# Optimization experiments

Hardware: AMD Instinct MI355X
Metric: run time of the kernel (lower is better)

The kernel has to match this reference:

```python
import jax, jax.numpy as jnp
import numpy as np

N_CONV = 3
FEAT = 128
N_RBF = 20
CUTOFF = 5.0
EPS = 1e-15
N_NODES = 10000
N_EDGES = 160000


def setup_inputs() -> dict:
    key = jax.random.key(0)
    ks = jax.random.split(key, 8)
    N, E = N_NODES, N_EDGES
    cg_xyz = jax.random.normal(ks[0], (N, 3), jnp.float32) * 2.0
    # Directed, self-loop-free edge list (both i<j and i>j present, so the
    # original make_directed() is a no-op on this data).
    src = jax.random.randint(ks[1], (E,), 0, N)
    off = jax.random.randint(ks[2], (E,), 1, N)
    CG_nbr_list = jnp.stack([src, (src + off) % N], axis=1)
    cg_s = jax.random.normal(ks[3], (N, FEAT), jnp.float32)
    s = 1.0 / np.sqrt(FEAT)
    # Per-conv-layer weights of ENMessageBlock: inv_dense = Dense(F->F, silu) + Dense(F->3F);
    # dist_embed = ExpNormalBasis(n_rbf) -> Dense(n_rbf->3F) * cosine envelope.
    W1 = jax.random.normal(ks[4], (N_CONV, FEAT, FEAT), jnp.float32) * s
    b1 = jnp.zeros((N_CONV, FEAT), jnp.float32)
    W2 = jax.random.normal(ks[5], (N_CONV, FEAT, 3 * FEAT), jnp.float32) * s
    b2 = jnp.zeros((N_CONV, 3 * FEAT), jnp.float32)
    Wr = jax.random.normal(ks[6], (N_CONV, N_RBF, 3 * FEAT), jnp.float32) / np.sqrt(N_RBF)
    br = jnp.zeros((N_CONV, 3 * FEAT), jnp.float32)
    return {"cg_xyz": cg_xyz, "CG_nbr_list": CG_nbr_list, "cg_s": cg_s,
            "W1": W1, "b1": b1, "W2": W2, "b2": b2, "Wr": Wr, "br": br}


def _expnorm_rbf(dist):
    # ExpNormalBasis: exp(-beta * (exp(-d) - mu)^2), mu in [exp(-cutoff), 1]
    mu = jnp.linspace(np.exp(-CUTOFF), 1.0, N_RBF, dtype=jnp.float32)
    beta = np.float32((2.0 / N_RBF * (1.0 - np.exp(-CUTOFF))) ** -2)
    return jnp.exp(-beta * (jnp.exp(-dist)[:, None] - mu) ** 2)  # (E, n_rbf)


def _cos_envelope(dist):
    return jnp.where(dist < CUTOFF, 0.5 * (jnp.cos(jnp.pi * dist / CUTOFF) + 1.0), 0.0)


def reference(cg_xyz, CG_nbr_list, cg_s, W1, b1, W2, b2, Wr, br):
    N = cg_s.shape[0]
    i, j = CG_nbr_list[:, 0], CG_nbr_list[:, 1]
    r_ij = cg_xyz[j] - cg_xyz[i]                      # (E, 3)
    dist = jnp.sqrt((r_ij ** 2 + EPS).sum(-1))        # (E,)
    unit = r_ij / dist[:, None]                        # (E, 3)
    rbf = _expnorm_rbf(dist)                           # (E, n_rbf) edge-invariant across layers
    env = _cos_envelope(dist)[:, None]                 # (E, 1)

    s_i = cg_s                                         # (N, F)
    v_i = jnp.zeros((N, FEAT, 3), cg_s.dtype)          # (N, F, 3)
    for l in range(N_CONV):
        phi = jax.nn.silu(s_i @ W1[l] + b1[l]) @ W2[l] + b2[l]   # (N, 3F)
        w_s = (rbf @ Wr[l] + br[l]) * env                         # (E, 3F)
        prod = phi[j] * w_s                                       # (E, 3F) gather + gate
        ds = prod[:, :FEAT]                                       # scalar message
        gate_v = prod[:, FEAT:2 * FEAT]                           # gates v_j
        gate_u = prod[:, 2 * FEAT:]                               # gates unit vector
        dv_ij = gate_u[:, :, None] * unit[:, None, :] + gate_v[:, :, None] * v_i[j]  # (E, F, 3)
        s_i = s_i + jax.ops.segment_sum(ds, i, num_segments=N)
        v_i = v_i + jax.ops.segment_sum(dv_ij, i, num_segments=N)
    return s_i, v_i
```

## Files before the change

### kernel.cpp

```cpp
#include <hip/hip_runtime.h>
#include <hip/hip_bf16.h>

#define NRBF 20
#define KAUG 32

typedef __attribute__((ext_vector_type(8))) short short8;
typedef __attribute__((ext_vector_type(4))) float float4v;
typedef __attribute__((ext_vector_type(2))) _Float16 half2v;
typedef __attribute__((ext_vector_type(8))) _Float16 half8v;
typedef unsigned short ushort_t;

union H8 { half8v v8; half2v v2[4]; };

__device__ __forceinline__ float bf2f(ushort_t u) {
    return __uint_as_float(((unsigned)u) << 16);
}
__device__ __forceinline__ ushort_t f2bf(float f) {
    unsigned u = __float_as_uint(f);
    u += 0x7FFF + ((u >> 16) & 1);
    return (ushort_t)(u >> 16);
}
__device__ __forceinline__ float ldin(const void* p, size_t idx, int isbf) {
    return isbf ? bf2f(((const ushort_t*)p)[idx]) : ((const float*)p)[idx];
}
__device__ __forceinline__ void stout(void* p, size_t idx, float v, int isbf) {
    if (isbf) ((ushort_t*)p)[idx] = f2bf(v);
    else      ((float*)p)[idx] = v;
}
__device__ __forceinline__ float dot2(half2v a, half2v b, float c) {
#if __has_builtin(__builtin_amdgcn_fdot2)
    return __builtin_amdgcn_fdot2(a, b, c, false);
#else
    return c + (float)a.x * (float)b.x + (float)a.y * (float)b.y;
#endif
}

__global__ void detect_kernel(const void* __restrict__ xyz, int* __restrict__ flag,
                              int* __restrict__ deg, int N) {
    int idx = blockIdx.x * blockDim.x + threadIdx.x;
    if (idx < N) deg[idx] = 0;
    if (blockIdx.x == 0 && threadIdx.x < 64) {
        const ushort_t* u = (const ushort_t*)xyz;
        unsigned e0 = (u[2 * threadIdx.x] >> 7) & 0xFF;
        unsigned long long bad = __ballot(e0 >= 0x90);
        if (threadIdx.x == 0) *flag = (__popcll(bad) > 2) ? 0 : 1;
    }
}

__global__ void prelude_kernel(const void* __restrict__ xyz, const int* __restrict__ nbr,
                               const void* __restrict__ cg_s,
                               const void* __restrict__ W1, const void* __restrict__ W2,
                               const void* __restrict__ Wr, const void* __restrict__ br,
                               float* __restrict__ s_acc, ushort_t* __restrict__ s_hi,
                               ushort_t* __restrict__ s_lo, int* __restrict__ deg,
                               ushort_t* __restrict__ B1hi, ushort_t* __restrict__ B1lo,
                               ushort_t* __restrict__ B2hi, ushort_t* __restrict__ B2lo,
                               _Float16* __restrict__ WrT,
                               int N128, int E, const int* __restrict__ flagp) {
    int isbf = *flagp;
    int idx = blockIdx.x * blockDim.x + threadIdx.x;
    if (idx < E) {
        int i = nbr[2 * idx], j = nbr[2 * idx + 1];
        float dx = ldin(xyz, 3 * j,     isbf) - ldin(xyz, 3 * i,     isbf);
        float dy = ldin(xyz, 3 * j + 1, isbf) - ldin(xyz, 3 * i + 1, isbf);
        float dz = ldin(xyz, 3 * j + 2, isbf) - ldin(xyz, 3 * i + 2, isbf);
        float dist = sqrtf(dx * dx + dy * dy + dz * dz + 3e-15f);
        if (dist < 5.0f) atomicAdd(&deg[i], 1);
    }
    if (idx < N128) {
        float v = ldin(cg_s, idx, isbf);
        s_acc[idx] = v;
        ushort_t hi = f2bf(v);
        s_hi[idx] = hi;
        s_lo[idx] = f2bf(v - bf2f(hi));
    }
    const int NW1 = 3 * 4 * 8 * 64;
    const int NW2 = 3 * 4 * 24 * 64;
    const int NWT = 3 * 384;
    if (idx < NW1) {
        int lane = idx & 63;
        int t = idx >> 6;
        int nt = t % 8; t /= 8;
        int ks = t % 4; int l = t / 4;
        int n = lane & 15, quad = lane >> 4;
        int col = nt * 16 + n;
        size_t base = (size_t)l * 128 * 128;
        size_t fo = (size_t)idx * 8;
        #pragma unroll
        for (int j = 0; j < 8; j++) {
            int k = ks * 32 + quad * 8 + j;
            float v = ldin(W1, base + (size_t)k * 128 + col, isbf);
            ushort_t hi = f2bf(v);
            B1hi[fo + j] = hi;
            B1lo[fo + j] = f2bf(v - bf2f(hi));
        }
    } else if (idx < NW1 + NW2) {
        int i2 = idx - NW1;
        int lane = i2 & 63;
        int t = i2 >> 6;
        int nt = t % 24; t /= 24;
        int ks = t % 4; int l = t / 4;
        int n = lane & 15, quad = lane >> 4;
        int col = nt * 16 + n;
        size_t base = (size_t)l * 128 * 384;
        size_t fo = (size_t)i2 * 8;
        #pragma unroll
        for (int j = 0; j < 8; j++) {
            int k = ks * 32 + quad * 8 + j;
            float v = ldin(W2, base + (size_t)k * 384 + col, isbf);
            ushort_t hi = f2bf(v);
            B2hi[fo + j] = hi;
            B2lo[fo + j] = f2bf(v - bf2f(hi));
        }
    } else if (idx < NW1 + NW2 + NWT) {
        int i2 = idx - NW1 - NW2;
        int l = i2 / 384, col = i2 % 384;
        _Float16* wt = WrT + ((size_t)l * 384 + col) * KAUG;
        #pragma unroll
        for (int k = 0; k < KAUG; k++) {
            float v = 0.f;
            if (k < NRBF) v = ldin(Wr, ((size_t)l * NRBF + k) * 384 + col, isbf);
            else if (k == NRBF) v = ldin(br, (size_t)l * 384 + col, isbf);
            wt[k] = (_Float16)v;
        }
    }
}

__global__ void scan_kernel(int* __restrict__ deg, int* __restrict__ rowptr, int N) {
    __shared__ int part[256];
    int t = threadIdx.x;
    int chunk = (N + 255) / 256;
    int lo = t * chunk, hi = min(lo + chunk, N);
    int s = 0;
    for (int i = lo; i < hi; i++) s += deg[i];
    part[t] = s;
    __syncthreads();
    for (int off = 1; off < 256; off <<= 1) {
        int v = (t >= off) ? part[t - off] : 0;
        __syncthreads();
        if (t >= off) part[t] += v;
        __syncthreads();
    }
    int base = (t == 0) ? 0 : part[t - 1];
    for (int i = lo; i < hi; i++) {
        rowptr[i] = base;
        int d = deg[i];
        deg[i] = base;
        base += d;
    }
    if (t == 0) rowptr[N] = part[255];
}

__global__ void pack_kernel(const void* __restrict__ xyz, const int* __restrict__ nbr,
                            int* __restrict__ cursor, int* __restrict__ jlist,
                            float4* __restrict__ upos, _Float16* __restrict__ rbfh,
                            int E, const int* __restrict__ flagp) {
    int isbf = *flagp;
    int e = blockIdx.x * blockDim.x + threadIdx.x;
    if (e >= E) return;
    int i = nbr[2 * e], j = nbr[2 * e + 1];
    float dx = ldin(xyz, 3 * j,     isbf) - ldin(xyz, 3 * i,     isbf);
    float dy = ldin(xyz, 3 * j + 1, isbf) - ldin(xyz, 3 * i + 1, isbf);
    float dz = ldin(xyz, 3 * j + 2, isbf) - ldin(xyz, 3 * i + 2, isbf);
    float dist = sqrtf(dx * dx + dy * dy + dz * dz + 3e-15f);
    if (!(dist < 5.0f)) return;
    constexpr float PI = 3.14159265358979323846f;
    float ev = 0.5f * (cosf(PI * dist * 0.2f) + 1.0f);
    int pos = atomicAdd(&cursor[i], 1);
    jlist[pos] = j;
    float inv = 1.0f / dist;
    upos[pos] = make_float4(dx * inv, dy * inv, dz * inv, ev);
    constexpr double EM5 = 0.006737946999085467;
    constexpr float MU0 = (float)EM5;
    constexpr float DMU = (float)((1.0 - EM5) / 19.0);
    constexpr float BETA = (float)(1.0 / ((0.1 * (1.0 - EM5)) * (0.1 * (1.0 - EM5))));
    float ed = expf(-dist);
    _Float16* rp = rbfh + (size_t)pos * KAUG;
    #pragma unroll
    for (int k = 0; k < NRBF; k++) {
        float dmu = ed - (MU0 + k * DMU);
        rp[k] = (_Float16)(ev * expf(-BETA * dmu * dmu));
    }
    rp[NRBF] = (_Float16)ev;
    #pragma unroll
    for (int k = NRBF + 1; k < 24; k++) rp[k] = (_Float16)0.f;
}

template <int ACT, int OUTMODE, int NTILES>
__global__ __launch_bounds__(256) void mfma_gemm(
    const ushort_t* __restrict__ Ahi, const ushort_t* __restrict__ Alo,
    const ushort_t* __restrict__ Bhi, const ushort_t* __restrict__ Blo,
    const void* __restrict__ bias, size_t biasoff,
    ushort_t* __restrict__ out_hi, ushort_t* __restrict__ out_lo,
    int M, const int* __restrict__ flagp) {
    constexpr int Ncols = NTILES * 16;
    int isbf = *flagp;
    int nt = blockIdx.x % NTILES;
    int bx = blockIdx.x / NTILES;
    int tid = threadIdx.x;
    int wave = tid >> 6, lane = tid & 63;
    int m = lane & 15, quad = lane >> 4;
    int brow = bx * 64 + wave * 16;
    int row = brow + m;
    float4v acc = {};
    short8 zero8 = {};
    #pragma unroll
    for (int ks = 0; ks < 4; ks++) {
        short8 ah = zero8, al = zero8;
        if (row < M) {
            size_t ao = (size_t)row * 128 + ks * 32 + quad * 8;
            ah = *reinterpret_cast<const short8*>(Ahi + ao);
            al = *reinterpret_cast<const short8*>(Alo + ao);
        }
        size_t fo = (((size_t)ks * NTILES + nt) * 64 + lane) * 8;
        short8 bh = *reinterpret_cast<const short8*>(Bhi + fo);
        acc = __builtin_amdgcn_mfma_f32_16x16x32_bf16(ah, bh, acc, 0, 0, 0);
        acc = __builtin_amdgcn_mfma_f32_16x16x32_bf16(al, bh, acc, 0, 0, 0);
        if (!isbf) {
            short8 bl = *reinterpret_cast<const short8*>(Blo + fo);
            acc = __builtin_amdgcn_mfma_f32_16x16x32_bf16(ah, bl, acc, 0, 0, 0);
        }
    }
    int col = nt * 16 + m;
    float bv = ldin(bias, biasoff + col, isbf);
    #pragma unroll
    for (int r = 0; r < 4; r++) {
        int orow = brow + quad * 4 + r;
        if (orow >= M) continue;
        float x = acc[r] + bv;
        if (ACT) x = x / (1.0f + expf(-x));
        size_t oo = (size_t)orow * Ncols + col;
        ushort_t h = f2bf(x);
        out_hi[oo] = h;
        if (OUTMODE == 0) out_lo[oo] = f2bf(x - bf2f(h));
    }
}

template <int L0, int LAST>
__global__ __launch_bounds__(128, 4) void node_kernel(
    const int* __restrict__ rowptr, const int* __restrict__ jlist,
    const float4* __restrict__ upos, const _Float16* __restrict__ rbfh,
    const _Float16* __restrict__ WrT,
    const ushort_t* __restrict__ phi,
    const float* __restrict__ v_old, const ushort_t* __restrict__ vh_old,
    float* __restrict__ s_acc, ushort_t* __restrict__ s_hi, ushort_t* __restrict__ s_lo,
    float* __restrict__ v_new, ushort_t* __restrict__ vh_new,
    void* __restrict__ out, int N, const int* __restrict__ flagp) {
    int isbf = *flagp;
    int tt = threadIdx.x;
    int node = blockIdx.x;

    H8 wcA[3], wcB[3], wcC[3];
    {
        const half8v* w0p = (const half8v*)(WrT + (size_t)tt * KAUG);
        const half8v* w1p = (const half8v*)(WrT + (size_t)(tt + 128) * KAUG);
        const half8v* w2p = (const half8v*)(WrT + (size_t)(tt + 256) * KAUG);
        #pragma unroll
        for (int q = 0; q < 3; q++) {
            wcA[q].v8 = w0p[q]; wcB[q].v8 = w1p[q]; wcC[q].v8 = w2p[q];
        }
    }
    int start = __builtin_amdgcn_readfirstlane(rowptr[node]);
    int end   = __builtin_amdgcn_readfirstlane(rowptr[node + 1]);

    float dsv = 0.f, ax = 0.f, ay = 0.f, az = 0.f;
    if (start < end) {
        int j_c = jlist[start];
        float4 u_c = upos[start];
        const half8v* rp = (const half8v*)(rbfh + (size_t)start * KAUG);
        H8 r0, r1, r2;
        r0.v8 = rp[0]; r1.v8 = rp[1]; r2.v8 = rp[2];
        size_t jb = (size_t)j_c * 384;
        ushort_t p0 = phi[jb + tt], p1 = phi[jb + 128 + tt], p2 = phi[jb + 256 + tt];
        ushort_t v0 = 0, v1 = 0, v2 = 0;
        if (!L0) {
            const ushort_t* vj = &vh_old[jb + (size_t)tt * 3];
            v0 = vj[0]; v1 = vj[1]; v2 = vj[2];
        }
        for (int k = start; k < end; k++) {
            int kn = (k + 1 < end) ? k + 1 : k;
            int j_n = jlist[kn];
            float4 u_n = upos[kn];
            const half8v* rpn = (const half8v*)(rbfh + (size_t)kn * KAUG);
            H8 n0, n1, n2;
            n0.v8 = rpn[0]; n1.v8 = rpn[1]; n2.v8 = rpn[2];
            size_t jbn = (size_t)j_n * 384;
            ushort_t q0 = phi[jbn + tt], q1 = phi[jbn + 128 + tt], q2 = phi[jbn + 256 + tt];
            ushort_t x0 = 0, x1 = 0, x2 = 0;
            if (!L0) {
                const ushort_t* vjn = &vh_old[jbn + (size_t)tt * 3];
                x0 = vjn[0]; x1 = vjn[1]; x2 = vjn[2];
            }
            float w0 = 0.f, w1 = 0.f, w2 = 0.f;
            #pragma unroll
            for (int q = 0; q < 3; q++) {
                const H8& rq = (q == 0) ? r0 : (q == 1) ? r1 : r2;
                #pragma unroll
                for (int p = 0; p < 4; p++) {
                    half2v pr = rq.v2[p];
                    w0 = dot2(pr, wcA[q].v2[p], w0);
                    w1 = dot2(pr, wcB[q].v2[p], w1);
                    w2 = dot2(pr, wcC[q].v2[p], w2);
                }
            }
            dsv += bf2f(p0) * w0;
            float gv = bf2f(p1) * w1;
            float gu = bf2f(p2) * w2;
            if (L0) {
                ax += gu * u_c.x; ay += gu * u_c.y; az += gu * u_c.z;
            } else {
                ax += gu * u_c.x + gv * bf2f(v0);
                ay += gu * u_c.y + gv * bf2f(v1);
                az += gu * u_c.z + gv * bf2f(v2);
            }
            u_c = u_n; r0 = n0; r1 = n1; r2 = n2;
            p0 = q0; p1 = q1; p2 = q2;
            v0 = x0; v1 = x1; v2 = x2;
        }
    }
    size_t so = (size_t)node * 128 + tt;
    float snew = s_acc[so] + dsv;
    size_t ib = (size_t)node * 384 + (size_t)tt * 3;
    float vx = L0 ? ax : v_old[ib]     + ax;
    float vy = L0 ? ay : v_old[ib + 1] + ay;
    float vz = L0 ? az : v_old[ib + 2] + az;
    if (LAST) {
        stout(out, so, snew, isbf);
        size_t ob = (size_t)N * 128 + ib;
        stout(out, ob,     vx, isbf);
        stout(out, ob + 1, vy, isbf);
        stout(out, ob + 2, vz, isbf);
    } else {
        s_acc[so] = snew;
        ushort_t hi = f2bf(snew);
        s_hi[so] = hi;
        s_lo[so] = f2bf(snew - bf2f(hi));
        v_new[ib] = vx; v_new[ib + 1] = vy; v_new[ib + 2] = vz;
        vh_new[ib]     = f2bf(vx);
        vh_new[ib + 1] = f2bf(vy);
        vh_new[ib + 2] = f2bf(vz);
    }
}

extern "C" void kernel_launch(void* const* d_in, const int* in_sizes, int n_in,
                              void* d_out, int out_size, void* d_ws, size_t ws_size,
                              hipStream_t stream) {
    const int N = in_sizes[0] / 3;
    const int E = in_sizes[1] / 2;
    const void* xyz  = d_in[0];
    const int*  nbr  = (const int*)d_in[1];
    const void* cg_s = d_in[2];
    const void* W1   = d_in[3];
    const void* b1   = d_in[4];
    const void* W2   = d_in[5];
    const void* b2   = d_in[6];
    const void* Wr   = d_in[7];
    const void* br   = d_in[8];

    size_t off = 0;
    auto alloc = [&](size_t bytes) -> char* {
        char* p = (char*)d_ws + off;
        off = (off + bytes + 63) & ~(size_t)63;
        return p;
    };
    int*       flag   = (int*)alloc(64);
    float*     s_acc  = (float*)alloc((size_t)N * 128 * 4);
    float*     vA     = (float*)alloc((size_t)N * 384 * 4);
    float*     vB     = (float*)alloc((size_t)N * 384 * 4);
    int*       rowptr = (int*)alloc((size_t)(N + 1) * 4);
    int*       deg    = (int*)alloc((size_t)N * 4);
    int*       jlist  = (int*)alloc((size_t)E * 4);
    float4*    upos   = (float4*)alloc((size_t)(E + 16) * 16);
    _Float16*  rbfh   = (_Float16*)alloc((size_t)(E + 16) * KAUG * 2);
    _Float16*  WrT    = (_Float16*)alloc((size_t)3 * 384 * KAUG * 2);
    ushort_t*  s_hi   = (ushort_t*)alloc((size_t)N * 128 * 2);
    ushort_t*  s_lo   = (ushort_t*)alloc((size_t)N * 128 * 2);
    ushort_t*  h_hi   = (ushort_t*)alloc((size_t)N * 128 * 2);
    ushort_t*  h_lo   = (ushort_t*)alloc((size_t)N * 128 * 2);
    ushort_t*  phi    = (ushort_t*)alloc((size_t)N * 384 * 2);
    ushort_t*  vhA    = (ushort_t*)alloc((size_t)N * 384 * 2);
    ushort_t*  vhB    = (ushort_t*)alloc((size_t)N * 384 * 2);
    ushort_t*  B1hi   = (ushort_t*)alloc((size_t)3 * 4 * 8 * 64 * 8 * 2);
    ushort_t*  B1lo   = (ushort_t*)alloc((size_t)3 * 4 * 8 * 64 * 8 * 2);
    ushort_t*  B2hi   = (ushort_t*)alloc((size_t)3 * 4 * 24 * 64 * 8 * 2);
    ushort_t*  B2lo   = (ushort_t*)alloc((size_t)3 * 4 * 24 * 64 * 8 * 2);

    detect_kernel<<<(N + 255) / 256, 256, 0, stream>>>(xyz, flag, deg, N);
    const int N128 = N * 128;
    const int pg = (max(E, N128) + 255) / 256;
    prelude_kernel<<<pg, 256, 0, stream>>>(xyz, nbr, cg_s, W1, W2, Wr, br,
                                           s_acc, s_hi, s_lo, deg,
                                           B1hi, B1lo, B2hi, B2lo, WrT,
                                           N128, E, flag);
    scan_kernel<<<1, 256, 0, stream>>>(deg, rowptr, N);
    pack_kernel<<<(E + 255) / 256, 256, 0, stream>>>(xyz, nbr, deg, jlist, upos,
                                                     rbfh, E, flag);

    const int gx = (N + 63) / 64;
    for (int l = 0; l < 3; l++) {
        mfma_gemm<1, 0, 8><<<gx * 8, 256, 0, stream>>>(
            s_hi, s_lo,
            B1hi + (size_t)l * 4 * 8 * 64 * 8, B1lo + (size_t)l * 4 * 8 * 64 * 8,
            b1, (size_t)l * 128, h_hi, h_lo, N, flag);
        mfma_gemm<0, 1, 24><<<gx * 24, 256, 0, stream>>>(
            h_hi, h_lo,
            B2hi + (size_t)l * 4 * 24 * 64 * 8, B2lo + (size_t)l * 4 * 24 * 64 * 8,
            b2, (size_t)l * 384, phi, (ushort_t*)nullptr, N, flag);
        const _Float16* wrt = WrT + (size_t)l * 384 * KAUG;
        if (l == 0) {
            node_kernel<1, 0><<<N, 128, 0, stream>>>(
                rowptr, jlist, upos, rbfh, wrt, phi,
                vA, vhA, s_acc, s_hi, s_lo, vA, vhA, d_out, N, flag);
        } else if (l == 1) {
            node_kernel<0, 0><<<N, 128, 0, stream>>>(
                rowptr, jlist, upos, rbfh, wrt, phi,
                vA, vhA, s_acc, s_hi, s_lo, vB, vhB, d_out, N, flag);
        } else {
            node_kernel<0, 1><<<N, 128, 0, stream>>>(
                rowptr, jlist, upos, rbfh, wrt, phi,
                vB, vhB, s_acc, s_hi, s_lo, vB, vhB, d_out, N, flag);
        }
    }
}
```

Before: 339.6 us.

## Fuse the two dense GEMMs, pack neighbor index into upos, and process two nodes per block

Result: slower. 347.3 us (+2.3%).

```diff
diff --git a/kernel.cpp b/kernel.cpp
--- a/kernel.cpp
+++ b/kernel.cpp
@@ -2,7 +2,7 @@
 #include <hip/hip_bf16.h>
 
 #define NRBF 20
-#define KAUG 32
+#define KAUG 24
 
 typedef __attribute__((ext_vector_type(8))) short short8;
 typedef __attribute__((ext_vector_type(4))) float float4v;
@@ -34,17 +34,12 @@
     return c + (float)a.x * (float)b.x + (float)a.y * (float)b.y;
 #endif
 }
-
-__global__ void detect_kernel(const void* __restrict__ xyz, int* __restrict__ flag,
-                              int* __restrict__ deg, int N) {
-    int idx = blockIdx.x * blockDim.x + threadIdx.x;
-    if (idx < N) deg[idx] = 0;
-    if (blockIdx.x == 0 && threadIdx.x < 64) {
-        const ushort_t* u = (const ushort_t*)xyz;
-        unsigned e0 = (u[2 * threadIdx.x] >> 7) & 0xFF;
-        unsigned long long bad = __ballot(e0 >= 0x90);
-        if (threadIdx.x == 0) *flag = (__popcll(bad) > 2) ? 0 : 1;
-    }
+__device__ __forceinline__ int detect_isbf(const void* xyz) {
+    const ushort_t* u = (const ushort_t*)xyz;
+    unsigned lane = threadIdx.x & 63;
+    unsigned e0 = (u[2 * lane] >> 7) & 0xFF;
+    unsigned long long bad = __ballot(e0 >= 0x90);
+    return (__popcll(bad) > 2) ? 0 : 1;
 }
 
 __global__ void prelude_kernel(const void* __restrict__ xyz, const int* __restrict__ nbr,
@@ -56,8 +51,8 @@
                                ushort_t* __restrict__ B1hi, ushort_t* __restrict__ B1lo,
                                ushort_t* __restrict__ B2hi, ushort_t* __restrict__ B2lo,
                                _Float16* __restrict__ WrT,
-                               int N128, int E, const int* __restrict__ flagp) {
-    int isbf = *flagp;
+                               int N128, int E) {
+    int isbf = detect_isbf(xyz);
     int idx = blockIdx.x * blockDim.x + threadIdx.x;
     if (idx < E) {
         int i = nbr[2 * idx], j = nbr[2 * idx + 1];
@@ -152,10 +147,10 @@
 }
 
 __global__ void pack_kernel(const void* __restrict__ xyz, const int* __restrict__ nbr,
-                            int* __restrict__ cursor, int* __restrict__ jlist,
+                            int* __restrict__ cursor,
                             float4* __restrict__ upos, _Float16* __restrict__ rbfh,
-                            int E, const int* __restrict__ flagp) {
-    int isbf = *flagp;
+                            int E) {
+    int isbf = detect_isbf(xyz);
     int e = blockIdx.x * blockDim.x + threadIdx.x;
     if (e >= E) return;
     int i = nbr[2 * e], j = nbr[2 * e + 1];
@@ -167,9 +162,8 @@
     constexpr float PI = 3.14159265358979323846f;
     float ev = 0.5f * (cosf(PI * dist * 0.2f) + 1.0f);
     int pos = atomicAdd(&cursor[i], 1);
-    jlist[pos] = j;
     float inv = 1.0f / dist;
-    upos[pos] = make_float4(dx * inv, dy * inv, dz * inv, ev);
+    upos[pos] = make_float4(dx * inv, dy * inv, dz * inv, __int_as_float(j));
     constexpr double EM5 = 0.006737946999085467;
     constexpr float MU0 = (float)EM5;
     constexpr float DMU = (float)((1.0 - EM5) / 19.0);
@@ -183,72 +177,114 @@
     }
     rp[NRBF] = (_Float16)ev;
     #pragma unroll
-    for (int k = NRBF + 1; k < 24; k++) rp[k] = (_Float16)0.f;
-}
-
-template <int ACT, int OUTMODE, int NTILES>
-__global__ __launch_bounds__(256) void mfma_gemm(
-    const ushort_t* __restrict__ Ahi, const ushort_t* __restrict__ Alo,
-    const ushort_t* __restrict__ Bhi, const ushort_t* __restrict__ Blo,
-    const void* __restrict__ bias, size_t biasoff,
-    ushort_t* __restrict__ out_hi, ushort_t* __restrict__ out_lo,
-    int M, const int* __restrict__ flagp) {
-    constexpr int Ncols = NTILES * 16;
-    int isbf = *flagp;
-    int nt = blockIdx.x % NTILES;
-    int bx = blockIdx.x / NTILES;
+    for (int k = NRBF + 1; k < KAUG; k++) rp[k] = (_Float16)0.f;
+}
+
+__global__ __launch_bounds__(256) void gemm12_kernel(
+    const void* __restrict__ xyz,
+    const ushort_t* __restrict__ s_hi, const ushort_t* __restrict__ s_lo,
+    const ushort_t* __restrict__ B1hi, const ushort_t* __restrict__ B1lo,
+    const void* __restrict__ b1, size_t b1off,
+    const ushort_t* __restrict__ B2hi, const ushort_t* __restrict__ B2lo,
+    const void* __restrict__ b2, size_t b2off,
+    ushort_t* __restrict__ phi, int M) {
+    int isbf = detect_isbf(xyz);
+    __shared__ ushort_t hhi[64][136];
+    __shared__ ushort_t hlo[64][136];
+    int yb = blockIdx.x % 6;
+    int bx = blockIdx.x / 6;
     int tid = threadIdx.x;
     int wave = tid >> 6, lane = tid & 63;
     int m = lane & 15, quad = lane >> 4;
-    int brow = bx * 64 + wave * 16;
-    int row = brow + m;
-    float4v acc = {};
+    int wr0 = wave * 16;
+    int brow = bx * 64;
+    int row = brow + wr0 + m;
     short8 zero8 = {};
-    #pragma unroll
-    for (int ks = 0; ks < 4; ks++) {
-        short8 ah = zero8, al = zero8;
-        if (row < M) {
-            size_t ao = (size_t)row * 128 + ks * 32 + quad * 8;
-            ah = *reinterpret_cast<const short8*>(Ahi + ao);
-            al = *reinterpret_cast<const short8*>(Alo + ao);
-        }
-        size_t fo = (((size_t)ks * NTILES + nt) * 64 + lane) * 8;
-        short8 bh = *reinterpret_cast<const short8*>(Bhi + fo);
-        acc = __builtin_amdgcn_mfma_f32_16x16x32_bf16(ah, bh, acc, 0, 0, 0);
-        acc = __builtin_amdgcn_mfma_f32_16x16x32_bf16(al, bh, acc, 0, 0, 0);
-        if (!isbf) {
-            short8 bl = *reinterpret_cast<const short8*>(Blo + fo);
-            acc = __builtin_amdgcn_mfma_f32_16x16x32_bf16(ah, bl, acc, 0, 0, 0);
-        }
-    }
-    int col = nt * 16 + m;
-    float bv = ldin(bias, biasoff + col, isbf);
-    #pragma unroll
-    for (int r = 0; r < 4; r++) {
-        int orow = brow + quad * 4 + r;
-        if (orow >= M) continue;
-        float x = acc[r] + bv;
-        if (ACT) x = x / (1.0f + expf(-x));
-        size_t oo = (size_t)orow * Ncols + col;
-        ushort_t h = f2bf(x);
-        out_hi[oo] = h;
-        if (OUTMODE == 0) out_lo[oo] = f2bf(x - bf2f(h));
+    {
+        float4v acc1[8] = {};
+        #pragma unroll
+        for (int ks = 0; ks < 4; ks++) {
+            short8 ah = zero8, al = zero8;
+            if (row < M) {
+                size_t ao = (size_t)row * 128 + ks * 32 + quad * 8;
+                ah = *reinterpret_cast<const short8*>(s_hi + ao);
+                al = *reinterpret_cast<const short8*>(s_lo + ao);
+            }
+            #pragma unroll
+            for (int nt = 0; nt < 8; nt++) {
+                size_t fo = (((size_t)ks * 8 + nt) * 64 + lane) * 8;
+                short8 bh = *reinterpret_cast<const short8*>(B1hi + fo);
+                acc1[nt] = __builtin_amdgcn_mfma_f32_16x16x32_bf16(ah, bh, acc1[nt], 0, 0, 0);
+                acc1[nt] = __builtin_amdgcn_mfma_f32_16x16x32_bf16(al, bh, acc1[nt], 0, 0, 0);
+                if (!isbf) {
+                    short8 bl = *reinterpret_cast<const short8*>(B1lo + fo);
+                    acc1[nt] = __builtin_amdgcn_mfma_f32_16x16x32_bf16(ah, bl, acc1[nt], 0, 0, 0);
+                }
+            }
+        }
+        #pragma unroll
+        for (int nt = 0; nt < 8; nt++) {
+            int col = nt * 16 + m;
+            float bv = ldin(b1, b1off + col, isbf);
+            #pragma unroll
+            for (int r = 0; r < 4; r++) {
+                int lrow = wr0 + quad * 4 + r;
+                float x = acc1[nt][r] + bv;
+                x = x / (1.0f + expf(-x));
+                ushort_t h = f2bf(x);
+                hhi[lrow][col] = h;
+                hlo[lrow][col] = f2bf(x - bf2f(h));
+            }
+        }
+    }
+    __syncthreads();
+    {
+        int ntg0 = yb * 4;
+        float4v acc2[4] = {};
+        #pragma unroll
+        for (int ks = 0; ks < 4; ks++) {
+            short8 ah = *reinterpret_cast<const short8*>(&hhi[wr0 + m][ks * 32 + quad * 8]);
+            short8 al = *reinterpret_cast<const short8*>(&hlo[wr0 + m][ks * 32 + quad * 8]);
+            #pragma unroll
+            for (int nt = 0; nt < 4; nt++) {
+                size_t fo = (((size_t)ks * 24 + ntg0 + nt) * 64 + lane) * 8;
+                short8 bh = *reinterpret_cast<const short8*>(B2hi + fo);
+                acc2[nt] = __builtin_amdgcn_mfma_f32_16x16x32_bf16(ah, bh, acc2[nt], 0, 0, 0);
+                acc2[nt] = __builtin_amdgcn_mfma_f32_16x16x32_bf16(al, bh, acc2[nt], 0, 0, 0);
+                if (!isbf) {
+                    short8 bl = *reinterpret_cast<const short8*>(B2lo + fo);
+                    acc2[nt] = __builtin_amdgcn_mfma_f32_16x16x32_bf16(ah, bl, acc2[nt], 0, 0, 0);
+                }
+            }
+        }
+        #pragma unroll
+        for (int nt = 0; nt < 4; nt++) {
+            int col = (ntg0 + nt) * 16 + m;
+            float bv = ldin(b2, b2off + col, isbf);
+            #pragma unroll
+            for (int r = 0; r < 4; r++) {
+                int orow = brow + wr0 + quad * 4 + r;
+                if (orow < M) phi[(size_t)orow * 384 + col] = f2bf(acc2[nt][r] + bv);
+            }
+        }
     }
 }
 
 template <int L0, int LAST>
-__global__ __launch_bounds__(128, 4) void node_kernel(
-    const int* __restrict__ rowptr, const int* __restrict__ jlist,
+__global__ __launch_bounds__(256, 4) void node_kernel(
+    const void* __restrict__ xyz,
+    const int* __restrict__ rowptr,
     const float4* __restrict__ upos, const _Float16* __restrict__ rbfh,
     const _Float16* __restrict__ WrT,
     const ushort_t* __restrict__ phi,
     const float* __restrict__ v_old, const ushort_t* __restrict__ vh_old,
     float* __restrict__ s_acc, ushort_t* __restrict__ s_hi, ushort_t* __restrict__ s_lo,
     float* __restrict__ v_new, ushort_t* __restrict__ vh_new,
-    void* __restrict__ out, int N, const int* __restrict__ flagp) {
-    int isbf = *flagp;
-    int tt = threadIdx.x;
-    int node = blockIdx.x;
+    void* __restrict__ out, int N) {
+    int isbf = detect_isbf(xyz);
+    int tt = threadIdx.x & 127;
+    int node = (blockIdx.x << 1) | (threadIdx.x >> 7);
+    if (node >= N) return;
 
     H8 wcA[3], wcB[3], wcC[3];
     {
@@ -265,8 +301,8 @@
 
     float dsv = 0.f, ax = 0.f, ay = 0.f, az = 0.f;
     if (start < end) {
-        int j_c = jlist[start];
         float4 u_c = upos[start];
+        int j_c = __builtin_amdgcn_readfirstlane(__float_as_int(u_c.w));
         const half8v* rp = (const half8v*)(rbfh + (size_t)start * KAUG);
         H8 r0, r1, r2;
         r0.v8 = rp[0]; r1.v8 = rp[1]; r2.v8 = rp[2];
@@ -279,8 +315,8 @@
         }
         for (int k = start; k < end; k++) {
             int kn = (k + 1 < end) ? k + 1 : k;
-            int j_n = jlist[kn];
             float4 u_n = upos[kn];
+            int j_n = __builtin_amdgcn_readfirstlane(__float_as_int(u_n.w));
             const half8v* rpn = (const half8v*)(rbfh + (size_t)kn * KAUG);
             H8 n0, n1, n2;
             n0.v8 = rpn[0]; n1.v8 = rpn[1]; n2.v8 = rpn[2];
@@ -363,20 +399,16 @@
         off = (off + bytes + 63) & ~(size_t)63;
         return p;
     };
-    int*       flag   = (int*)alloc(64);
     float*     s_acc  = (float*)alloc((size_t)N * 128 * 4);
     float*     vA     = (float*)alloc((size_t)N * 384 * 4);
     float*     vB     = (float*)alloc((size_t)N * 384 * 4);
     int*       rowptr = (int*)alloc((size_t)(N + 1) * 4);
     int*       deg    = (int*)alloc((size_t)N * 4);
-    int*       jlist  = (int*)alloc((size_t)E * 4);
     float4*    upos   = (float4*)alloc((size_t)(E + 16) * 16);
     _Float16*  rbfh   = (_Float16*)alloc((size_t)(E + 16) * KAUG * 2);
     _Float16*  WrT    = (_Float16*)alloc((size_t)3 * 384 * KAUG * 2);
     ushort_t*  s_hi   = (ushort_t*)alloc((size_t)N * 128 * 2);
     ushort_t*  s_lo   = (ushort_t*)alloc((size_t)N * 128 * 2);
-    ushort_t*  h_hi   = (ushort_t*)alloc((size_t)N * 128 * 2);
-    ushort_t*  h_lo   = (ushort_t*)alloc((size_t)N * 128 * 2);
     ushort_t*  phi    = (ushort_t*)alloc((size_t)N * 384 * 2);
     ushort_t*  vhA    = (ushort_t*)alloc((size_t)N * 384 * 2);
     ushort_t*  vhB    = (ushort_t*)alloc((size_t)N * 384 * 2);
@@ -385,40 +417,38 @@
     ushort_t*  B2hi   = (ushort_t*)alloc((size_t)3 * 4 * 24 * 64 * 8 * 2);
     ushort_t*  B2lo   = (ushort_t*)alloc((size_t)3 * 4 * 24 * 64 * 8 * 2);
 
-    detect_kernel<<<(N + 255) / 256, 256, 0, stream>>>(xyz, flag, deg, N);
+    hipMemsetAsync(deg, 0, (size_t)N * sizeof(int), stream);
     const int N128 = N * 128;
     const int pg = (max(E, N128) + 255) / 256;
     prelude_kernel<<<pg, 256, 0, stream>>>(xyz, nbr, cg_s, W1, W2, Wr, br,
                                            s_acc, s_hi, s_lo, deg,
                                            B1hi, B1lo, B2hi, B2lo, WrT,
-                                           N128, E, flag);
+                                           N128, E);
     scan_kernel<<<1, 256, 0, stream>>>(deg, rowptr, N);
-    pack_kernel<<<(E + 255) / 256, 256, 0, stream>>>(xyz, nbr, deg, jlist, upos,
-                                                     rbfh, E, flag);
+    pack_kernel<<<(E + 255) / 256, 256, 0, stream>>>(xyz, nbr, deg, upos, rbfh, E);
 
     const int gx = (N + 63) / 64;
+    const int ng = (N + 1) / 2;
     for (int l = 0; l < 3; l++) {
-        mfma_gemm<1, 0, 8><<<gx * 8, 256, 0, stream>>>(
-            s_hi, s_lo,
+        gemm12_kernel<<<gx * 6, 256, 0, stream>>>(
+            xyz, s_hi, s_lo,
             B1hi + (size_t)l * 4 * 8 * 64 * 8, B1lo + (size_t)l * 4 * 8 * 64 * 8,
-            b1, (size_t)l * 128, h_hi, h_lo, N, flag);
-        mfma_gemm<0, 1, 24><<<gx * 24, 256, 0, stream>>>(
-            h_hi, h_lo,
+            b1, (size_t)l * 128,
             B2hi + (size_t)l * 4 * 24 * 64 * 8, B2lo + (size_t)l * 4 * 24 * 64 * 8,
-            b2, (size_t)l * 384, phi, (ushort_t*)nullptr, N, flag);
+            b2, (size_t)l * 384, phi, N);
         const _Float16* wrt = WrT + (size_t)l * 384 * KAUG;
         if (l == 0) {
-            node_kernel<1, 0><<<N, 128, 0, stream>>>(
-                rowptr, jlist, upos, rbfh, wrt, phi,
-                vA, vhA, s_acc, s_hi, s_lo, vA, vhA, d_out, N, flag);
+            node_kernel<1, 0><<<ng, 256, 0, stream>>>(
+                xyz, rowptr, upos, rbfh, wrt, phi,
+                vA, vhA, s_acc, s_hi, s_lo, vA, vhA, d_out, N);
         } else if (l == 1) {
-            node_kernel<0, 0><<<N, 128, 0, stream>>>(
-                rowptr, jlist, upos, rbfh, wrt, phi,
-                vA, vhA, s_acc, s_hi, s_lo, vB, vhB, d_out, N, flag);
+            node_kernel<0, 0><<<ng, 256, 0, stream>>>(
+                xyz, rowptr, upos, rbfh, wrt, phi,
+                vA, vhA, s_acc, s_hi, s_lo, vB, vhB, d_out, N);
         } else {
-            node_kernel<0, 1><<<N, 128, 0, stream>>>(
-                rowptr, jlist, upos, rbfh, wrt, phi,
-                vB, vhB, s_acc, s_hi, s_lo, vB, vhB, d_out, N, flag);
-        }
-    }
-}
+            node_kernel<0, 1><<<ng, 256, 0, stream>>>(
+                xyz, rowptr, upos, rbfh, wrt, phi,
+                vB, vhB, s_acc, s_hi, s_lo, vB, vhB, d_out, N);
+        }
+    }
+}
```
